# Optimization experiments

Measured on AMD Instinct MI355X. Metric: run time of the kernel, lower is better.

Reference implementation:

```python
import jax, jax.numpy as jnp
import numpy as np

N_NODES = 50000
N_EDGES = 800000
N_GRAPHS = 256
IN_DIM, HID = 300, 256
C1, C2, C3 = 16, 64, 256


def setup_inputs() -> dict:
    key = jax.random.key(0)
    ks = jax.random.split(key, 16)
    inp = {
        "x": jax.random.normal(ks[0], (N_NODES, IN_DIM), dtype=jnp.float32),
        "edge_index": jax.random.randint(ks[1], (2, N_EDGES), 0, N_NODES, dtype=jnp.int64),
        "batch": jnp.sort(jax.random.randint(ks[2], (N_NODES,), 0, N_GRAPHS, dtype=jnp.int64)),
    }
    def lin(k, fan_in, fan_out):
        s = 1.0 / np.sqrt(fan_in)
        kw, kb = jax.random.split(k)
        return (jax.random.uniform(kw, (fan_in, fan_out), minval=-s, maxval=s, dtype=jnp.float32),
                jax.random.uniform(kb, (fan_out,), minval=-s, maxval=s, dtype=jnp.float32))
    inp["W1"], inp["b1"] = lin(ks[3], IN_DIM, HID)
    inp["W2"], inp["b2"] = lin(ks[4], HID, HID)
    inp["W3"], inp["b3"] = lin(ks[5], HID, HID)
    inp["Wc1"], inp["bc1"] = lin(ks[6], HID, C1)
    inp["Wc2"], inp["bc2"] = lin(ks[7], HID + C1, C2)
    inp["Wc3"], inp["bc3"] = lin(ks[8], HID + C2, C3)
    return inp


def reference(x, edge_index, batch, W1, b1, W2, b2, W3, b3, Wc1, bc1, Wc2, bc2, Wc3, bc3):
    N = x.shape[0]
    loop = jnp.arange(N, dtype=edge_index.dtype)
    src = jnp.concatenate([edge_index[0], loop])   # source nodes (+ self-loops)
    dst = jnp.concatenate([edge_index[1], loop])   # target nodes (+ self-loops)
    # symmetric GCN normalization: deg^{-1/2}[src] * deg^{-1/2}[dst], deg incl self-loops
    deg = jax.ops.segment_sum(jnp.ones(src.shape, x.dtype), dst, num_segments=N)
    dinv = jnp.where(deg > 0, jax.lax.rsqrt(deg), 0.0)
    norm = dinv[src] * dinv[dst]                   # [E+N]

    def gcn_conv(h, W, b):
        h = h @ W                                  # transform first (PyG order)
        msg = h[src] * norm[:, None]               # gather + scale
        return jax.ops.segment_sum(msg, dst, num_segments=N) + b  # scatter-add

    h = jax.nn.relu(gcn_conv(x, W1, b1))           # dropout = identity (eval)
    h = jax.nn.relu(gcn_conv(h, W2, b2))
    h = gcn_conv(h, W3, b3)

    # global mean pool over graphs
    cnt = jax.ops.segment_sum(jnp.ones((N,), x.dtype), batch, num_segments=N_GRAPHS)
    pooled = jax.ops.segment_sum(h, batch, num_segments=N_GRAPHS) / jnp.maximum(cnt, 1.0)[:, None]

    l1 = pooled @ Wc1 + bc1
    p1 = jax.nn.softmax(l1, axis=1)
    l2 = jnp.concatenate([pooled, p1], axis=1) @ Wc2 + bc2
    p2 = jax.nn.softmax(l2, axis=1)
    l3 = jnp.concatenate([pooled, p2], axis=1) @ Wc3 + bc3
    return (l1, l2, l3)
```

## Files before the change

kernel.cpp:

```cpp
#include <hip/hip_runtime.h>
#include <hip/hip_bf16.h>

#define N_NODES 50000
#define N_EDGES 800000
#define N_GRAPHS 256
#define IN_DIM 300
#define HID 256
#define ROWS_PAD 50048

typedef __bf16 bf16x8 __attribute__((ext_vector_type(8)));
typedef short  s16x8  __attribute__((ext_vector_type(8)));
typedef short  s16x4  __attribute__((ext_vector_type(4)));
typedef float  f32x4  __attribute__((ext_vector_type(4)));
typedef float  f32x2  __attribute__((ext_vector_type(2)));

static __device__ __forceinline__ ushort f2bf(float f) {
    union { float f; uint u; } v; v.f = f;
    uint u = v.u;
    uint r = (u + 0x7fffu + ((u >> 16) & 1u)) >> 16;
    return (ushort)r;
}
static __device__ __forceinline__ float bf2f(ushort b) {
    union { uint u; float f; } v; v.u = ((uint)b) << 16;
    return v.f;
}
static __device__ __forceinline__ unsigned char f2fp8(float f) {
    int pk = __builtin_amdgcn_cvt_pk_fp8_f32(f, f, 0, 0);
    return (unsigned char)(pk & 0xff);
}


__global__ void count_deg(const int* __restrict__ dst, int* __restrict__ cnt, int E) {
    int e = blockIdx.x * 256 + threadIdx.x;
    if (e < E) atomicAdd(&cnt[dst[e]], 1);
}

__global__ void scan1(const int* __restrict__ cnt, int* __restrict__ rp,
                      int* __restrict__ bsums, float* __restrict__ dinv, int n) {
    __shared__ int s[256];
    int i = blockIdx.x * 256 + threadIdx.x;
    int v = (i < n) ? cnt[i] : 0;
    if (i < n) dinv[i] = rsqrtf((float)(v + 1));
    s[threadIdx.x] = v;
    __syncthreads();
    for (int off = 1; off < 256; off <<= 1) {
        int t = (threadIdx.x >= off) ? s[threadIdx.x - off] : 0;
        __syncthreads();
        s[threadIdx.x] += t;
        __syncthreads();
    }
    if (i < n) rp[i] = s[threadIdx.x] - v;
    if (threadIdx.x == 255) bsums[blockIdx.x] = s[255];
}

__global__ void scan2(int* __restrict__ bsums, int nb) {
    __shared__ int s[256];
    int v = (threadIdx.x < nb) ? bsums[threadIdx.x] : 0;
    s[threadIdx.x] = v;
    __syncthreads();
    for (int off = 1; off < 256; off <<= 1) {
        int t = (threadIdx.x >= off) ? s[threadIdx.x - off] : 0;
        __syncthreads();
        s[threadIdx.x] += t;
        __syncthreads();
    }
    if (threadIdx.x < nb) bsums[threadIdx.x] = s[threadIdx.x] - v;
}

__global__ void scan3(int* __restrict__ rp, int* __restrict__ cursor,
                      const int* __restrict__ bsums, int n) {
    int i = blockIdx.x * 256 + threadIdx.x;
    if (i < n) {
        int v = rp[i] + bsums[blockIdx.x];
        rp[i] = v;
        cursor[i] = v;
    }
}

__global__ void fill_csr(const int* __restrict__ src, const int* __restrict__ dst,
                         int* __restrict__ cursor, int* __restrict__ col, int E) {
    int e = blockIdx.x * 256 + threadIdx.x;
    if (e < E) {
        int d = dst[e];
        int p = atomicAdd(&cursor[d], 1);
        col[p] = src[e];
    }
}


__global__ __launch_bounds__(256) void transpose_w3(const float* __restrict__ W1,
                                                    const float* __restrict__ W2,
                                                    const float* __restrict__ W3,
                                                    ushort* __restrict__ Wt1,
                                                    ushort* __restrict__ Wt2,
                                                    ushort* __restrict__ Wt3) {
    int b = blockIdx.x;
    int n = threadIdx.x;
    if (b < 320) {
        int k = b;
        Wt1[(size_t)n * 320 + k] = (k < IN_DIM) ? f2bf(W1[(size_t)k * 256 + n]) : (ushort)0;
    } else if (b < 576) {
        int k = b - 320;
        Wt2[(size_t)n * 256 + k] = f2bf(W2[(size_t)k * 256 + n]);
    } else {
        int k = b - 576;
        Wt3[(size_t)n * 256 + k] = f2bf(W3[(size_t)k * 256 + n]);
    }
}


template <int KA, int KACT, bool AF32>
__global__ __launch_bounds__(256) void gemm_bf16(const void* __restrict__ Ap,
                                                 const ushort* __restrict__ Bt,
                                                 unsigned char* __restrict__ C, int M) {
    __shared__ ushort As[64 * 40];
    __shared__ ushort Bs[256 * 40];

    int t = threadIdx.x;
    int wave = t >> 6, lane = t & 63, quad = lane >> 4, l16 = lane & 15;
    int r0 = blockIdx.x * 64;
    int arow = t >> 2, aseg = t & 3;

    f32x4 acc[4][4] = {};

    for (int kc = 0; kc < KA; kc += 32) {
        if constexpr (AF32) {
            const float* Af = (const float*)Ap;
            int row = r0 + arow;
            int kb = kc + aseg * 8;
            ushort tmp[8];
            if (row < M && kb + 7 < KACT) {
                f32x4 f0 = *(const f32x4*)(Af + (size_t)row * KACT + kb);
                f32x4 f1 = *(const f32x4*)(Af + (size_t)row * KACT + kb + 4);
#pragma unroll
                for (int i = 0; i < 4; ++i) { tmp[i] = f2bf(f0[i]); tmp[4 + i] = f2bf(f1[i]); }
            } else {
#pragma unroll
                for (int i = 0; i < 8; ++i) {
                    int kk = kb + i;
                    tmp[i] = (row < M && kk < KACT) ? f2bf(Af[(size_t)row * KACT + kk]) : (ushort)0;
                }
            }
            *(s16x8*)(As + arow * 40 + aseg * 8) = *(const s16x8*)tmp;
        } else {
            const ushort* A = (const ushort*)Ap;
            *(s16x8*)(As + arow * 40 + aseg * 8) =
                *(const s16x8*)(A + (size_t)(r0 + arow) * KA + kc + aseg * 8);
        }
#pragma unroll
        for (int s = 0; s < 4; ++s) {
            *(s16x8*)(Bs + t * 40 + s * 8) =
                *(const s16x8*)(Bt + (size_t)t * KA + kc + s * 8);
        }
        __syncthreads();

        bf16x8 a[4], b[4];
#pragma unroll
        for (int i = 0; i < 4; ++i)
            a[i] = __builtin_bit_cast(bf16x8, *(const s16x8*)(As + (i * 16 + l16) * 40 + quad * 8));
#pragma unroll
        for (int j = 0; j < 4; ++j)
            b[j] = __builtin_bit_cast(bf16x8, *(const s16x8*)(Bs + (wave * 64 + j * 16 + l16) * 40 + quad * 8));
#pragma unroll
        for (int i = 0; i < 4; ++i)
#pragma unroll
            for (int j = 0; j < 4; ++j)
                acc[i][j] = __builtin_amdgcn_mfma_f32_16x16x32_bf16(a[i], b[j], acc[i][j], 0, 0, 0);
        __syncthreads();
    }

#pragma unroll
    for (int i = 0; i < 4; ++i) {
        int rowb = r0 + i * 16 + quad * 4;
#pragma unroll
        for (int r = 0; r < 4; ++r) {
            if (rowb + r < M) {
#pragma unroll
                for (int j = 0; j < 4; ++j) {
                    int colv = wave * 64 + j * 16 + l16;
                    C[(size_t)(rowb + r) * 256 + colv] = f2fp8(acc[i][j][r]);
                }
            }
        }
    }
}


__global__ __launch_bounds__(256) void aggregate_fp8(const unsigned char* __restrict__ z,
                                                     ushort* __restrict__ out,
                                                     const int* __restrict__ rp,
                                                     const int* __restrict__ cnt,
                                                     const int* __restrict__ col,
                                                     const float* __restrict__ dinv,
                                                     const float* __restrict__ bias, int relu) {
    const uint* zu = (const uint*)z;
    int t = threadIdx.x;
    int wave = __builtin_amdgcn_readfirstlane(t >> 6);
    int lane = t & 63;
    int n = blockIdx.x * 4 + wave;
    int start = rp[n];
    int c = cnt[n];
    float dv = dinv[n];

    float a0 = 0.f, a1 = 0.f, a2 = 0.f, a3 = 0.f;

    int j = 0;
    for (; j + 4 <= c; j += 4) {
        int r0 = col[start + j], r1 = col[start + j + 1];
        int r2 = col[start + j + 2], r3 = col[start + j + 3];
        float w0 = dinv[r0], w1 = dinv[r1], w2 = dinv[r2], w3 = dinv[r3];
        uint v0 = zu[(size_t)r0 * 64 + lane];
        uint v1 = zu[(size_t)r1 * 64 + lane];
        uint v2 = zu[(size_t)r2 * 64 + lane];
        uint v3 = zu[(size_t)r3 * 64 + lane];
        f32x2 p, q;
        p = __builtin_amdgcn_cvt_pk_f32_fp8(v0, 0); q = __builtin_amdgcn_cvt_pk_f32_fp8(v0, 1);
        a0 += w0 * p[0]; a1 += w0 * p[1]; a2 += w0 * q[0]; a3 += w0 * q[1];
        p = __builtin_amdgcn_cvt_pk_f32_fp8(v1, 0); q = __builtin_amdgcn_cvt_pk_f32_fp8(v1, 1);
        a0 += w1 * p[0]; a1 += w1 * p[1]; a2 += w1 * q[0]; a3 += w1 * q[1];
        p = __builtin_amdgcn_cvt_pk_f32_fp8(v2, 0); q = __builtin_amdgcn_cvt_pk_f32_fp8(v2, 1);
        a0 += w2 * p[0]; a1 += w2 * p[1]; a2 += w2 * q[0]; a3 += w2 * q[1];
        p = __builtin_amdgcn_cvt_pk_f32_fp8(v3, 0); q = __builtin_amdgcn_cvt_pk_f32_fp8(v3, 1);
        a0 += w3 * p[0]; a1 += w3 * p[1]; a2 += w3 * q[0]; a3 += w3 * q[1];
    }
    for (; j < c; ++j) {
        int r = col[start + j];
        float w = dinv[r];
        uint v = zu[(size_t)r * 64 + lane];
        f32x2 p = __builtin_amdgcn_cvt_pk_f32_fp8(v, 0);
        f32x2 q = __builtin_amdgcn_cvt_pk_f32_fp8(v, 1);
        a0 += w * p[0]; a1 += w * p[1]; a2 += w * q[0]; a3 += w * q[1];
    }

    uint vs = zu[(size_t)n * 64 + lane];
    f32x2 sp = __builtin_amdgcn_cvt_pk_f32_fp8(vs, 0);
    f32x2 sq = __builtin_amdgcn_cvt_pk_f32_fp8(vs, 1);
    float sv[4] = {sp[0], sp[1], sq[0], sq[1]};
    f32x4 bv = *(const f32x4*)(bias + lane * 4);
    ushort o[4];
#pragma unroll
    for (int i = 0; i < 4; ++i) {
        float acc = (i == 0 ? a0 : i == 1 ? a1 : i == 2 ? a2 : a3);
        float r = dv * (acc + dv * sv[i]) + bv[i];
        if (relu) r = fmaxf(r, 0.f);
        o[i] = f2bf(r);
    }
    *(s16x4*)(out + (size_t)n * HID + (size_t)lane * 4) = *(const s16x4*)o;
}


__global__ __launch_bounds__(256) void pool_sum(const ushort* __restrict__ h,
                                                const int* __restrict__ batch,
                                                float* __restrict__ psum, int n) {
    int f = threadIdx.x;
    int r0 = blockIdx.x * 64;
    int rend = min(r0 + 64, n);
    if (r0 >= n) return;
    int g = batch[r0];
    float acc = 0.f;
    for (int r = r0; r < rend; ++r) {
        int gr = batch[r];
        if (gr != g) {
            atomicAdd(&psum[g * HID + f], acc);
            acc = 0.f;
            g = gr;
        }
        acc += bf2f(h[(size_t)r * HID + f]);
    }
    atomicAdd(&psum[g * HID + f], acc);
}


__global__ __launch_bounds__(256) void head_k(const float* __restrict__ psum,
                                              const int* __restrict__ batch, int n,
                                              const float* __restrict__ Wc1, const float* __restrict__ bc1,
                                              const float* __restrict__ Wc2, const float* __restrict__ bc2,
                                              const float* __restrict__ Wc3, const float* __restrict__ bc3,
                                              float* __restrict__ out) {
    int g = blockIdx.x;
    int t = threadIdx.x;
    __shared__ float pr[256];
    __shared__ float l1s[16], p1s[16];
    __shared__ float l2s[64], p2s[64];
    int lo = 0, hi = n;
    while (lo < hi) { int mid = (lo + hi) >> 1; if (batch[mid] < g) lo = mid + 1; else hi = mid; }
    int start = lo;
    lo = start; hi = n;
    while (lo < hi) { int mid = (lo + hi) >> 1; if (batch[mid] < g + 1) lo = mid + 1; else hi = mid; }
    int c = lo - start;
    float inv_c = 1.f / (float)max(c, 1);
    pr[t] = psum[g * 256 + t] * inv_c;
    __syncthreads();
    if (t < 16) {
        float a = bc1[t];
        for (int k = 0; k < 256; ++k) a += pr[k] * Wc1[k * 16 + t];
        l1s[t] = a;
        out[g * 16 + t] = a;
    }
    __syncthreads();
    if (t == 0) {
        float m = -1e30f;
        for (int j = 0; j < 16; ++j) m = fmaxf(m, l1s[j]);
        float s = 0.f;
        for (int j = 0; j < 16; ++j) { float e = expf(l1s[j] - m); p1s[j] = e; s += e; }
        float inv = 1.f / s;
        for (int j = 0; j < 16; ++j) p1s[j] *= inv;
    }
    __syncthreads();
    if (t < 64) {
        float a = bc2[t];
        for (int k = 0; k < 256; ++k) a += pr[k] * Wc2[k * 64 + t];
        for (int k = 0; k < 16; ++k) a += p1s[k] * Wc2[(256 + k) * 64 + t];
        l2s[t] = a;
        out[4096 + g * 64 + t] = a;
    }
    __syncthreads();
    if (t == 0) {
        float m = -1e30f;
        for (int j = 0; j < 64; ++j) m = fmaxf(m, l2s[j]);
        float s = 0.f;
        for (int j = 0; j < 64; ++j) { float e = expf(l2s[j] - m); p2s[j] = e; s += e; }
        float inv = 1.f / s;
        for (int j = 0; j < 64; ++j) p2s[j] *= inv;
    }
    __syncthreads();
    {
        float a = bc3[t];
        for (int k = 0; k < 256; ++k) a += pr[k] * Wc3[k * 256 + t];
        for (int k = 0; k < 64; ++k) a += p2s[k] * Wc3[(256 + k) * 256 + t];
        out[4096 + 16384 + g * 256 + t] = a;
    }
}


extern "C" void kernel_launch(void* const* d_in, const int* in_sizes, int n_in,
                              void* d_out, int out_size, void* d_ws, size_t ws_size,
                              hipStream_t stream) {
    const float* x    = (const float*)d_in[0];
    const int*   ei   = (const int*)d_in[1];
    const int*   batch= (const int*)d_in[2];
    const float* W1 = (const float*)d_in[3];  const float* b1 = (const float*)d_in[4];
    const float* W2 = (const float*)d_in[5];  const float* b2 = (const float*)d_in[6];
    const float* W3 = (const float*)d_in[7];  const float* b3 = (const float*)d_in[8];
    const float* Wc1= (const float*)d_in[9];  const float* bc1= (const float*)d_in[10];
    const float* Wc2= (const float*)d_in[11]; const float* bc2= (const float*)d_in[12];
    const float* Wc3= (const float*)d_in[13]; const float* bc3= (const float*)d_in[14];
    float* out = (float*)d_out;

    const int N = N_NODES, E = N_EDGES, G = N_GRAPHS;

    char* ws = (char*)d_ws;
    size_t off = 0;
    auto alloc = [&](size_t bytes) -> void* {
        void* p = ws + off;
        off = (off + bytes + 255) & ~(size_t)255;
        return p;
    };
    unsigned char* z = (unsigned char*)alloc((size_t)ROWS_PAD * HID);
    ushort* hb   = (ushort*)alloc((size_t)ROWS_PAD * HID * 2);
    ushort* Wt1  = (ushort*)alloc((size_t)256 * 320 * 2);
    ushort* Wt2  = (ushort*)alloc((size_t)256 * 256 * 2);
    ushort* Wt3  = (ushort*)alloc((size_t)256 * 256 * 2);
    int*   cnt    = (int*)alloc((size_t)N * 4);
    int*   rp     = (int*)alloc((size_t)N * 4);
    int*   cursor = (int*)alloc((size_t)N * 4);
    float* dinv   = (float*)alloc((size_t)N * 4);
    int*   col    = (int*)alloc((size_t)E * 4);
    float* psum   = (float*)alloc((size_t)G * HID * 4);
    int*   bsums  = (int*)alloc(256 * 4);
    (void)ws_size;

    const int* src = ei;
    const int* dst = ei + E;

    hipMemsetAsync(cnt, 0, (size_t)N * 4, stream);
    hipMemsetAsync(psum, 0, (size_t)G * HID * 4, stream);
    count_deg<<<(E + 255) / 256, 256, 0, stream>>>(dst, cnt, E);
    const int NB = (N + 255) / 256;
    scan1<<<NB, 256, 0, stream>>>(cnt, rp, bsums, dinv, N);
    scan2<<<1, 256, 0, stream>>>(bsums, NB);
    scan3<<<NB, 256, 0, stream>>>(rp, cursor, bsums, N);
    fill_csr<<<(E + 255) / 256, 256, 0, stream>>>(src, dst, cursor, col, E);

    transpose_w3<<<832, 256, 0, stream>>>(W1, W2, W3, Wt1, Wt2, Wt3);

    const int MB = (N + 63) / 64;
    gemm_bf16<320, IN_DIM, true><<<MB, 256, 0, stream>>>(x, Wt1, z, N);
    aggregate_fp8<<<N / 4, 256, 0, stream>>>(z, hb, rp, cnt, col, dinv, b1, 1);
    gemm_bf16<256, 256, false><<<MB, 256, 0, stream>>>(hb, Wt2, z, N);
    aggregate_fp8<<<N / 4, 256, 0, stream>>>(z, hb, rp, cnt, col, dinv, b2, 1);
    gemm_bf16<256, 256, false><<<MB, 256, 0, stream>>>(hb, Wt3, z, N);
    aggregate_fp8<<<N / 4, 256, 0, stream>>>(z, hb, rp, cnt, col, dinv, b3, 0);

    pool_sum<<<MB, 256, 0, stream>>>(hb, batch, psum, N);
    head_k<<<G, 256, 0, stream>>>(psum, batch, N, Wc1, bc1, Wc2, bc2, Wc3, bc3, out);
}
```

Measured before the change: 443.0 us.

## Retile node GEMM to 128-row blocks with 64-wide K chunks and slab LDS layout

Replaces the 64-row GEMM with a 128-row-per-block version that loads 64 K elements per iteration. Shared memory is stored in a k-slab-major layout (8-element slabs per row) instead of a padded row layout. Each wave now computes an 8x4 tile of MFMA accumulators, so every B fragment is reused across twice as many rows. Out-of-range rows are handled by clamping reads and by relying on buffers padded to ROWS_PAD. The trade-off is fewer blocks (about 391 on a 256-CU part) and higher register pressure per thread.

```diff
diff --git a/kernel.cpp b/kernel.cpp
--- a/kernel.cpp
+++ b/kernel.cpp
@@ -109,78 +109,85 @@
 }
 
 
-template <int KA, int KACT, bool AF32>
-__global__ __launch_bounds__(256) void gemm_bf16(const void* __restrict__ Ap,
-                                                 const ushort* __restrict__ Bt,
-                                                 unsigned char* __restrict__ C, int M) {
-    __shared__ ushort As[64 * 40];
-    __shared__ ushort Bs[256 * 40];
+template <int KP, int KACT, bool AF32>
+__global__ __launch_bounds__(256, 2) void gemm_v2(const void* __restrict__ Ap,
+                                                  const ushort* __restrict__ Bt,
+                                                  unsigned char* __restrict__ C, int M) {
+    __shared__ __align__(16) ushort As[8 * 128 * 8];
+    __shared__ __align__(16) ushort Bs[8 * 256 * 8];
 
     int t = threadIdx.x;
     int wave = t >> 6, lane = t & 63, quad = lane >> 4, l16 = lane & 15;
-    int r0 = blockIdx.x * 64;
-    int arow = t >> 2, aseg = t & 3;
-
-    f32x4 acc[4][4] = {};
-
-    for (int kc = 0; kc < KA; kc += 32) {
-        if constexpr (AF32) {
-            const float* Af = (const float*)Ap;
-            int row = r0 + arow;
-            int kb = kc + aseg * 8;
-            ushort tmp[8];
-            if (row < M && kb + 7 < KACT) {
-                f32x4 f0 = *(const f32x4*)(Af + (size_t)row * KACT + kb);
-                f32x4 f1 = *(const f32x4*)(Af + (size_t)row * KACT + kb + 4);
-#pragma unroll
-                for (int i = 0; i < 4; ++i) { tmp[i] = f2bf(f0[i]); tmp[4 + i] = f2bf(f1[i]); }
+    int r0 = blockIdx.x * 128;
+    int arow = t & 127;
+    int ahalf = t >> 7;
+
+    f32x4 acc[8][4] = {};
+
+    for (int kc = 0; kc < KP; kc += 64) {
+#pragma unroll
+        for (int i = 0; i < 8; ++i) {
+            *(s16x8*)(Bs + i * 2048 + t * 8) =
+                *(const s16x8*)(Bt + (size_t)t * KP + kc + i * 8);
+        }
+#pragma unroll
+        for (int i = 0; i < 4; ++i) {
+            int ks = 2 * i + ahalf;
+            int kg = kc + ks * 8;
+            if constexpr (AF32) {
+                const float* Af = (const float*)Ap;
+                int rg = r0 + arow; if (rg >= M) rg = M - 1;
+                ushort tmp[8];
+                if (kg + 8 <= KACT) {
+                    f32x4 f0 = *(const f32x4*)(Af + (size_t)rg * KACT + kg);
+                    f32x4 f1 = *(const f32x4*)(Af + (size_t)rg * KACT + kg + 4);
+#pragma unroll
+                    for (int j = 0; j < 4; ++j) { tmp[j] = f2bf(f0[j]); tmp[4 + j] = f2bf(f1[j]); }
+                } else if (kg < KACT) {
+                    f32x4 f0 = *(const f32x4*)(Af + (size_t)rg * KACT + kg);
+#pragma unroll
+                    for (int j = 0; j < 4; ++j) { tmp[j] = f2bf(f0[j]); tmp[4 + j] = 0; }
+                } else {
+#pragma unroll
+                    for (int j = 0; j < 8; ++j) tmp[j] = 0;
+                }
+                *(s16x8*)(As + ks * 1024 + arow * 8) = *(const s16x8*)tmp;
             } else {
-#pragma unroll
-                for (int i = 0; i < 8; ++i) {
-                    int kk = kb + i;
-                    tmp[i] = (row < M && kk < KACT) ? f2bf(Af[(size_t)row * KACT + kk]) : (ushort)0;
-                }
+                const ushort* A = (const ushort*)Ap;
+                *(s16x8*)(As + ks * 1024 + arow * 8) =
+                    *(const s16x8*)(A + (size_t)(r0 + arow) * KP + kg);
             }
-            *(s16x8*)(As + arow * 40 + aseg * 8) = *(const s16x8*)tmp;
-        } else {
-            const ushort* A = (const ushort*)Ap;
-            *(s16x8*)(As + arow * 40 + aseg * 8) =
-                *(const s16x8*)(A + (size_t)(r0 + arow) * KA + kc + aseg * 8);
         }
-#pragma unroll
-        for (int s = 0; s < 4; ++s) {
-            *(s16x8*)(Bs + t * 40 + s * 8) =
-                *(const s16x8*)(Bt + (size_t)t * KA + kc + s * 8);
+        __syncthreads();
+
+#pragma unroll
+        for (int ks = 0; ks < 2; ++ks) {
+            bf16x8 b[4];
+#pragma unroll
+            for (int ct = 0; ct < 4; ++ct)
+                b[ct] = __builtin_bit_cast(bf16x8,
+                    *(const s16x8*)(Bs + (ks * 4 + quad) * 2048 + (wave * 64 + ct * 16 + l16) * 8));
+#pragma unroll
+            for (int rt = 0; rt < 8; ++rt) {
+                bf16x8 a = __builtin_bit_cast(bf16x8,
+                    *(const s16x8*)(As + (ks * 4 + quad) * 1024 + (rt * 16 + l16) * 8));
+#pragma unroll
+                for (int ct = 0; ct < 4; ++ct)
+                    acc[rt][ct] = __builtin_amdgcn_mfma_f32_16x16x32_bf16(a, b[ct], acc[rt][ct], 0, 0, 0);
+            }
         }
         __syncthreads();
-
-        bf16x8 a[4], b[4];
-#pragma unroll
-        for (int i = 0; i < 4; ++i)
-            a[i] = __builtin_bit_cast(bf16x8, *(const s16x8*)(As + (i * 16 + l16) * 40 + quad * 8));
-#pragma unroll
-        for (int j = 0; j < 4; ++j)
-            b[j] = __builtin_bit_cast(bf16x8, *(const s16x8*)(Bs + (wave * 64 + j * 16 + l16) * 40 + quad * 8));
-#pragma unroll
-        for (int i = 0; i < 4; ++i)
-#pragma unroll
-            for (int j = 0; j < 4; ++j)
-                acc[i][j] = __builtin_amdgcn_mfma_f32_16x16x32_bf16(a[i], b[j], acc[i][j], 0, 0, 0);
-        __syncthreads();
-    }
-
-#pragma unroll
-    for (int i = 0; i < 4; ++i) {
-        int rowb = r0 + i * 16 + quad * 4;
-#pragma unroll
-        for (int r = 0; r < 4; ++r) {
-            if (rowb + r < M) {
-#pragma unroll
-                for (int j = 0; j < 4; ++j) {
-                    int colv = wave * 64 + j * 16 + l16;
-                    C[(size_t)(rowb + r) * 256 + colv] = f2fp8(acc[i][j][r]);
-                }
-            }
+    }
+
+#pragma unroll
+    for (int rt = 0; rt < 8; ++rt) {
+        int rowb = r0 + rt * 16 + quad * 4;
+#pragma unroll
+        for (int ct = 0; ct < 4; ++ct) {
+            int col = wave * 64 + ct * 16 + l16;
+#pragma unroll
+            for (int i = 0; i < 4; ++i)
+                C[(size_t)(rowb + i) * 256 + col] = f2fp8(acc[rt][ct][i]);
         }
     }
 }
@@ -384,14 +391,14 @@
 
     transpose_w3<<<832, 256, 0, stream>>>(W1, W2, W3, Wt1, Wt2, Wt3);
 
-    const int MB = (N + 63) / 64;
-    gemm_bf16<320, IN_DIM, true><<<MB, 256, 0, stream>>>(x, Wt1, z, N);
+    const int GB = ROWS_PAD / 128;
+    gemm_v2<320, IN_DIM, true><<<GB, 256, 0, stream>>>(x, Wt1, z, N);
     aggregate_fp8<<<N / 4, 256, 0, stream>>>(z, hb, rp, cnt, col, dinv, b1, 1);
-    gemm_bf16<256, 256, false><<<MB, 256, 0, stream>>>(hb, Wt2, z, N);
+    gemm_v2<256, 256, false><<<GB, 256, 0, stream>>>(hb, Wt2, z, N);
     aggregate_fp8<<<N / 4, 256, 0, stream>>>(z, hb, rp, cnt, col, dinv, b2, 1);
-    gemm_bf16<256, 256, false><<<MB, 256, 0, stream>>>(hb, Wt3, z, N);
+    gemm_v2<256, 256, false><<<GB, 256, 0, stream>>>(hb, Wt3, z, N);
     aggregate_fp8<<<N / 4, 256, 0, stream>>>(z, hb, rp, cnt, col, dinv, b3, 0);
 
-    pool_sum<<<MB, 256, 0, stream>>>(hb, batch, psum, N);
+    pool_sum<<<ROWS_PAD / 64, 256, 0, stream>>>(hb, batch, psum, N);
     head_k<<<G, 256, 0, stream>>>(psum, batch, N, Wc1, bc1, Wc2, bc2, Wc3, bc3, out);
 }
```

New measurement: 453.0 us. 1.02x slower.
